# Kernel tuning notes

Hardware: AMD Instinct MI355X
Metric: run time of the kernel (lower is better)

The kernel has to match this reference:

```python
import jax, jax.numpy as jnp
import numpy as np

NUM_TOKEN = 1024
IN_DIM = 512
OUT_DIM = 512
E = 1024          # expansion_factor * in_token_dims
S = 128
EPS = 1e-5
SQRT_S = float(np.sqrt(S))


def _rope_seq(x):
    """RoPE over axis 1 (sequence), last axis is feature dim. x: [B, L, ..., D]."""
    L = x.shape[1]
    half = x.shape[-1] // 2
    pos = jnp.arange(L, dtype=jnp.float32)
    inv_freq = 10000.0 ** (jnp.arange(half, dtype=jnp.float32) / half)
    sinusoid = pos[:, None] * inv_freq[None, :]          # [L, half]
    bshape = (1, L) + (1,) * (x.ndim - 3) + (half,)
    sin = jnp.sin(sinusoid).reshape(bshape)
    cos = jnp.cos(sinusoid).reshape(bshape)
    x1, x2 = jnp.split(x, 2, axis=-1)
    return jnp.concatenate([x1 * cos - x2 * sin, x2 * cos + x1 * sin], axis=-1)


def setup_inputs() -> dict:
    key = jax.random.key(0)
    ks = jax.random.split(key, 8)
    B = 32
    x = jax.random.normal(ks[0], (B, NUM_TOKEN, IN_DIM), jnp.float32)
    uv_w = jax.random.normal(ks[1], (2 * E + S, IN_DIM), jnp.float32) / np.sqrt(IN_DIM)
    o_w = jax.random.normal(ks[2], (OUT_DIM, E), jnp.float32) / np.sqrt(E)
    gamma = jax.random.uniform(ks[3], (2, S), jnp.float32)
    beta = jax.random.uniform(ks[4], (2, S), jnp.float32)
    w = jax.random.uniform(ks[5], (2 * NUM_TOKEN - 1,), jnp.float32)
    g = jnp.ones((1,), jnp.float32)                       # ScaleNorm gain
    res_scale = jnp.ones((IN_DIM,), jnp.float32)
    layer_scale = jnp.ones((OUT_DIM,), jnp.float32)
    return dict(x=x, uv_w=uv_w, o_w=o_w, gamma=gamma, beta=beta, w=w,
                g=g, res_scale=res_scale, layer_scale=layer_scale)


def reference(x, uv_w, o_w, gamma, beta, w, g, res_scale, layer_scale):
    B, L, D = x.shape
    # ScaleNorm
    norm = jnp.linalg.norm(x, axis=-1, keepdims=True) * (D ** -0.5)
    xn = x / jnp.maximum(norm, EPS) * g
    # shift mixing (time shift: first half channels shifted right by 1 token)
    xs, xp = jnp.split(xn, 2, axis=-1)
    xs = jnp.pad(xs, ((0, 0), (1, 0), (0, 0)))[:, :L, :]
    xn = jnp.concatenate([xs, xp], axis=-1)
    # uv projection + SiLU, then split into u, v, base
    uv = jax.nn.silu(xn @ uv_w.T)                         # [B, L, 2E+S]
    u, v, base = jnp.split(uv, [E, 2 * E], axis=-1)
    # per-head affine then RoPE
    base = base[:, :, None, :] * gamma[None, None] + beta  # [B, L, 2, S]
    base = _rope_seq(base)
    q, k = base[:, :, 0, :], base[:, :, 1, :]
    qk = jnp.einsum('bls,bms->blm', q, k)                 # [B, L, L]
    # structure-mode relative position bias: bias[i, j] = w[j - i + L - 1]
    idx = jnp.arange(L)[None, :] - jnp.arange(L)[:, None] + (L - 1)
    qk = qk + w[idx][None]
    kernel = jnp.square(jax.nn.relu(qk / SQRT_S))
    out = u * jnp.einsum('blm,bme->ble', kernel, v)       # gated quadratic attn
    out = out @ o_w.T                                     # [B, L, OUT_DIM]
    return x * res_scale + out * layer_scale
```

## Files before the change

kernel.cpp:

```cpp
#include <hip/hip_runtime.h>
#include <hip/hip_bf16.h>
#include <math.h>

typedef unsigned short u16;
typedef __bf16 bf16x8 __attribute__((ext_vector_type(8)));
typedef float f32x4 __attribute__((ext_vector_type(4)));

#define NB 32
#define LSEQ 1024
#define DIN 512
#define EDIM 1024
#define SDIM 128
#define NTOK (NB * LSEQ)
#define NUV 2176
#define CHUNK 16

#define AS1 __attribute__((address_space(1)))
#define AS3 __attribute__((address_space(3)))

__device__ __forceinline__ u16 f2bf(float f) {
  unsigned u = __builtin_bit_cast(unsigned, f);
  u += 0x7fffu + ((u >> 16) & 1u);
  return (u16)(u >> 16);
}
__device__ __forceinline__ float bf2f(u16 h) {
  unsigned u = ((unsigned)h) << 16;
  return __builtin_bit_cast(float, u);
}
__device__ __forceinline__ float fast_silu(float x) {
  float t = __builtin_amdgcn_exp2f(-1.44269504088896f * x);
  return x * __builtin_amdgcn_rcpf(1.0f + t);
}


__global__ __launch_bounds__(256) void k_f32_to_bf16(const float* __restrict__ in,
                                                     u16* __restrict__ out, int n4) {
  int i = blockIdx.x * 256 + threadIdx.x;
  if (i < n4) {
    float4 f = ((const float4*)in)[i];
    ushort4 o;
    o.x = f2bf(f.x); o.y = f2bf(f.y); o.z = f2bf(f.z); o.w = f2bf(f.w);
    ((ushort4*)out)[i] = o;
  }
}

__global__ __launch_bounds__(256) void k_normshift(const float* __restrict__ x,
                                                   const float* __restrict__ g,
                                                   u16* __restrict__ xn2) {
  int t = blockIdx.x;
  int l = t & (LSEQ - 1);
  float2 v = ((const float2*)(x + (size_t)t * DIN))[threadIdx.x];
  float ss = v.x * v.x + v.y * v.y;
  for (int o = 32; o > 0; o >>= 1) ss += __shfl_down(ss, o, 64);
  __shared__ float p[4];
  if ((threadIdx.x & 63) == 0) p[threadIdx.x >> 6] = ss;
  __syncthreads();
  float s = p[0] + p[1] + p[2] + p[3];
  float norm = sqrtf(s * (1.0f / (float)DIN));
  float inv = g[0] / fmaxf(norm, 1e-5f);
  int d = threadIdx.x * 2;
  ushort2 ob; ob.x = f2bf(v.x * inv); ob.y = f2bf(v.y * inv);
  if (d >= 256) {
    *(ushort2*)(xn2 + (size_t)t * DIN + d) = ob;
  } else {
    if (l < LSEQ - 1) *(ushort2*)(xn2 + (size_t)(t + 1) * DIN + d) = ob;
    if (l == 0) { ushort2 z = {0, 0}; *(ushort2*)(xn2 + (size_t)t * DIN + d) = z; }
  }
}

__global__ __launch_bounds__(256) void k_rope_table(float* __restrict__ sin_t,
                                                    float* __restrict__ cos_t) {
  int idx = blockIdx.x * 256 + threadIdx.x;
  int l = idx >> 6, j = idx & 63;
  double freq = pow(10000.0, (double)j / 64.0);
  float arg = (float)l * (float)freq;
  double a = (double)arg;
  sin_t[idx] = (float)sin(a);
  cos_t[idx] = (float)cos(a);
}

__global__ __launch_bounds__(256) void k_qkbuild(const u16* __restrict__ base,
                                                 const float* __restrict__ gamma,
                                                 const float* __restrict__ beta,
                                                 const float* __restrict__ sin_t,
                                                 const float* __restrict__ cos_t,
                                                 u16* __restrict__ q, u16* __restrict__ k) {
  int idx = blockIdx.x * 256 + threadIdx.x;
  int t = idx >> 6, j = idx & 63;
  int l = t & (LSEQ - 1);
  float b1 = bf2f(base[(size_t)t * SDIM + j]);
  float b2 = bf2f(base[(size_t)t * SDIM + j + 64]);
  float s = sin_t[l * 64 + j], c = cos_t[l * 64 + j];
  {
    float y1 = b1 * gamma[j] + beta[j];
    float y2 = b2 * gamma[64 + j] + beta[64 + j];
    q[(size_t)t * SDIM + j]      = f2bf(y1 * c - y2 * s);
    q[(size_t)t * SDIM + j + 64] = f2bf(y2 * c + y1 * s);
  }
  {
    float y1 = b1 * gamma[128 + j] + beta[128 + j];
    float y2 = b2 * gamma[192 + j] + beta[192 + j];
    k[(size_t)t * SDIM + j]      = f2bf(y1 * c - y2 * s);
    k[(size_t)t * SDIM + j + 64] = f2bf(y2 * c + y1 * s);
  }
}


__device__ __forceinline__ void stage128x32(const u16* g, int ld, u16* l, int tid) {
  int r = tid >> 2;
  int c = ((tid & 3) ^ ((tid >> 3) & 3)) * 8;
  const u16* g0 = g + (size_t)r * ld + c;
  const u16* g1 = g + (size_t)(r + 64) * ld + c;
  u16* l0 = l + tid * 8;
  u16* l1 = l + tid * 8 + 2048;
  __builtin_amdgcn_global_load_lds((AS1 unsigned int*)g0, (AS3 unsigned int*)l0, 16, 0, 0);
  __builtin_amdgcn_global_load_lds((AS1 unsigned int*)g1, (AS3 unsigned int*)l1, 16, 0, 0);
}

__device__ __forceinline__ void gemm_core(const u16* A, const u16* B, int K,
                                          int lda, int ldb,
                                          u16* sA, u16* sB, f32x4 acc[4][4]) {
  const int tid = threadIdx.x;
  const int lane = tid & 63;
  const int wid = tid >> 6;
  const int wr = wid >> 1, wc = wid & 1;
  const int fr = lane & 15, kg = lane >> 4;
  const int ks = (kg ^ ((fr >> 1) & 3)) * 8;
  const u16* sa_base = sA + (wr * 64 + fr) * 32 + ks;
  const u16* sb_base = sB + (wc * 64 + fr) * 32 + ks;
  for (int k0 = 0; k0 < K; k0 += 32) {
    stage128x32(A + k0, lda, sA, tid);
    stage128x32(B + k0, ldb, sB, tid);
    __syncthreads();
    bf16x8 a[4], b[4];
#pragma unroll
    for (int i = 0; i < 4; ++i) a[i] = *(const bf16x8*)(sa_base + i * 16 * 32);
#pragma unroll
    for (int i = 0; i < 4; ++i) b[i] = *(const bf16x8*)(sb_base + i * 16 * 32);
#pragma unroll
    for (int m = 0; m < 4; ++m)
#pragma unroll
      for (int n = 0; n < 4; ++n)
        acc[m][n] = __builtin_amdgcn_mfma_f32_16x16x32_bf16(a[m], b[n], acc[m][n], 0, 0, 0);
    __syncthreads();
  }
}


#define GROW_A(s) (wr * 128 + (s) * 32 + wc * 8)
#define GROW_B(s) (wid * 32 + (s) * 8)

#define STG_PAIR(s, At2, Bt2, dA, dB)                                              \
  do {                                                                             \
    __builtin_amdgcn_global_load_lds(                                              \
        (AS1 unsigned int*)((At2) + (size_t)(GROW_A(s) + srow) * lda + scol),      \
        (AS3 unsigned int*)((dA) + GROW_A(s) * 64), 16, 0, 0);                     \
    __builtin_amdgcn_global_load_lds(                                              \
        (AS1 unsigned int*)((Bt2) + (size_t)(GROW_B(s) + srow) * ldb + scol),      \
        (AS3 unsigned int*)((dB) + GROW_B(s) * 64), 16, 0, 0);                     \
  } while (0)

#define RD_A(dst, cbuf, q)                                                         \
  do {                                                                             \
    _Pragma("unroll") for (int r_ = 0; r_ < 2; ++r_)                               \
    _Pragma("unroll") for (int h_ = 0; h_ < 2; ++h_)                               \
      dst[r_][h_] = *(const bf16x8*)((cbuf) + (wr * 128 + (q) * 32 + r_ * 16 + fr) * 64 + \
                                     (((h_ * 4 + kg) ^ fr7) * 8));                 \
  } while (0)

#define RD_B(cbuf)                                                                 \
  do {                                                                             \
    _Pragma("unroll") for (int n_ = 0; n_ < 4; ++n_)                               \
    _Pragma("unroll") for (int h_ = 0; h_ < 2; ++h_)                               \
      breg[n_][h_] = *(const bf16x8*)((cbuf) + (wc * 64 + n_ * 16 + fr) * 64 +     \
                                      (((h_ * 4 + kg) ^ fr7) * 8));                \
  } while (0)

#define MFMA16(s, areg)                                                            \
  do {                                                                             \
    __builtin_amdgcn_s_setprio(1);                                                 \
    _Pragma("unroll") for (int r_ = 0; r_ < 2; ++r_)                               \
    _Pragma("unroll") for (int n_ = 0; n_ < 4; ++n_)                               \
    _Pragma("unroll") for (int h_ = 0; h_ < 2; ++h_)                               \
      acc[(s) * 2 + r_][n_] = __builtin_amdgcn_mfma_f32_16x16x32_bf16(             \
          areg[r_][h_], breg[n_][h_], acc[(s) * 2 + r_][n_], 0, 0, 0);             \
    __builtin_amdgcn_s_setprio(0);                                                 \
  } while (0)

#define BAR_FENCE()                                                                \
  do { __builtin_amdgcn_s_barrier(); asm volatile("" ::: "memory"); } while (0)

__device__ __forceinline__ void gemm256p_core(const u16* __restrict__ A, int lda,
                                              const u16* __restrict__ B, int ldb,
                                              int K, u16* smem, f32x4 (&acc)[8][4]) {
  const int tid = threadIdx.x;
  const int lane = tid & 63, wid = tid >> 6;
  const int wr = wid >> 2, wc = wid & 3;
  const int fr = lane & 15, kg = lane >> 4, fr7 = fr & 7;
  const int srow = lane >> 3;
  const int scol = ((lane & 7) ^ srow) * 8;
  u16* cA = smem;
  u16* cB = smem + 16384;
  u16* nA = smem + 32768;
  u16* nB = smem + 49152;
  const int nt = K >> 6;

#pragma unroll
  for (int s = 0; s < 4; ++s) STG_PAIR(s, A, B, cA, cB);
#pragma unroll
  for (int s = 0; s < 4; ++s) STG_PAIR(s, A + 64, B + 64, nA, nB);
  asm volatile("s_waitcnt vmcnt(8)" ::: "memory");
  BAR_FENCE();

  bf16x8 breg[4][2], ac[2][2], an[2][2];
  RD_B(cB);
  RD_A(ac, cA, 0);

  for (int t = 0; t < nt; ++t) {
    const bool st = (t + 2) < nt;
    const u16* At2 = A + (size_t)(t + 2) * 64;
    const u16* Bt2 = B + (size_t)(t + 2) * 64;
    MFMA16(0, ac);
    RD_A(an, cA, 1);
    BAR_FENCE();
    if (st) STG_PAIR(0, At2, Bt2, cA, cB);
    MFMA16(1, an);
    RD_A(ac, cA, 2);
    BAR_FENCE();
    if (st) STG_PAIR(1, At2, Bt2, cA, cB);
    MFMA16(2, ac);
    RD_A(an, cA, 3);
    BAR_FENCE();
    if (st) STG_PAIR(2, At2, Bt2, cA, cB);
    MFMA16(3, an);
    if (st) asm volatile("s_waitcnt vmcnt(6)" ::: "memory");
    else    asm volatile("s_waitcnt vmcnt(0)" ::: "memory");
    BAR_FENCE();
    if (st) STG_PAIR(3, At2, Bt2, cA, cB);
    { u16* tp = cA; cA = nA; nA = tp; tp = cB; cB = nB; nB = tp; }
    if (t + 1 < nt) { RD_B(cB); RD_A(ac, cA, 0); }
  }
}


__global__ __launch_bounds__(512, 2) void k_gemm_uv(const u16* __restrict__ xn2,
                                                    const u16* __restrict__ wbf,
                                                    u16* __restrict__ u, u16* __restrict__ vt,
                                                    u16* __restrict__ base) {
  __shared__ __align__(16) u16 smem[65536];
  f32x4 acc[8][4] = {};
  int bid = blockIdx.x;
  int xcd = bid & 7;
  int off = bid >> 3;
  int m0 = (xcd * 16 + off / 9) * 256;
  int n0 = (off % 9) * 256;
  gemm256p_core(xn2 + (size_t)m0 * DIN, DIN, wbf + (size_t)n0 * DIN, DIN, DIN, smem, acc);
  int lane = threadIdx.x & 63, wid = threadIdx.x >> 6;
  int wr = wid >> 2, wc = wid & 3;
  int cb = n0 + wc * 64 + (lane & 15);
  int rb = m0 + wr * 128 + (lane >> 4) * 4;
  if (n0 < EDIM) {
#pragma unroll
    for (int mm = 0; mm < 8; ++mm)
#pragma unroll
      for (int n = 0; n < 4; ++n) {
        int c = cb + n * 16;
#pragma unroll
        for (int j = 0; j < 4; ++j) {
          int r = rb + mm * 16 + j;
          u[(size_t)r * EDIM + c] = f2bf(fast_silu(acc[mm][n][j]));
        }
      }
  } else if (n0 < 2 * EDIM) {
    int b = m0 >> 10;
    u16* vtb = vt + (size_t)b * (EDIM * LSEQ);
#pragma unroll
    for (int mm = 0; mm < 8; ++mm) {
      int l0 = (rb + mm * 16) & (LSEQ - 1);
#pragma unroll
      for (int n = 0; n < 4; ++n) {
        int e = cb + n * 16 - EDIM;
        ushort4 o;
        o.x = f2bf(fast_silu(acc[mm][n][0]));
        o.y = f2bf(fast_silu(acc[mm][n][1]));
        o.z = f2bf(fast_silu(acc[mm][n][2]));
        o.w = f2bf(fast_silu(acc[mm][n][3]));
        *(ushort4*)(vtb + (size_t)e * LSEQ + l0) = o;
      }
    }
  } else if (wc < 2) {
#pragma unroll
    for (int mm = 0; mm < 8; ++mm)
#pragma unroll
      for (int n = 0; n < 4; ++n) {
        int c = cb + n * 16 - 2 * EDIM;
#pragma unroll
        for (int j = 0; j < 4; ++j) {
          int r = rb + mm * 16 + j;
          base[(size_t)r * SDIM + c] = f2bf(fast_silu(acc[mm][n][j]));
        }
      }
  }
}

__global__ __launch_bounds__(256) void k_gemm_qk(const u16* __restrict__ q,
                                                 const u16* __restrict__ k,
                                                 const float* __restrict__ w,
                                                 u16* __restrict__ scores) {
  __shared__ __align__(16) u16 sA[4096];
  __shared__ __align__(16) u16 sB[4096];
  f32x4 acc[4][4] = {};
  int bid = blockIdx.x;
  int xcd = bid & 7;
  int off = bid >> 3;
  int b = xcd * 2 + (off >> 6);
  int t = off & 63;
  int m0 = (t >> 3) * 128, n0 = (t & 7) * 128;
  gemm_core(q + (size_t)(b * LSEQ + m0) * SDIM, k + (size_t)(b * LSEQ + n0) * SDIM,
            SDIM, SDIM, SDIM, sA, sB, acc);
  int lane = threadIdx.x & 63, wid = threadIdx.x >> 6;
  int wr = wid >> 1, wc = wid & 1;
  int cb = n0 + wc * 64 + (lane & 15);
  int rb = m0 + wr * 64 + (lane >> 4) * 4;
  const float inv_sqrt_s = 0.08838834764831845f;
  u16* sc_b = scores + (size_t)b * LSEQ * LSEQ;
#pragma unroll
  for (int m = 0; m < 4; ++m)
#pragma unroll
    for (int n = 0; n < 4; ++n) {
      int c = cb + n * 16;
#pragma unroll
      for (int j = 0; j < 4; ++j) {
        int r = rb + m * 16 + j;
        float val = (acc[m][n][j] + w[c - r + (LSEQ - 1)]) * inv_sqrt_s;
        val = fmaxf(val, 0.0f);
        sc_b[(size_t)r * LSEQ + c] = f2bf(val * val);
      }
    }
}

__global__ __launch_bounds__(512, 2) void k_gemm_pv(const u16* __restrict__ scores,
                                                    const u16* __restrict__ vt,
                                                    u16* u_io) {
  __shared__ __align__(16) u16 smem[65536];
  f32x4 acc[8][4] = {};
  int bid = blockIdx.x;
  int xcd = bid & 7;
  int off = bid >> 3;
  int b = xcd * 2 + (off >> 4);
  int t = off & 15;
  int m0 = (t >> 2) * 256, n0 = (t & 3) * 256;
  gemm256p_core(scores + (size_t)b * LSEQ * LSEQ + (size_t)m0 * LSEQ, LSEQ,
                vt + (size_t)b * LSEQ * EDIM + (size_t)n0 * LSEQ, LSEQ,
                LSEQ, smem, acc);
  int lane = threadIdx.x & 63, wid = threadIdx.x >> 6;
  int wr = wid >> 2, wc = wid & 3;
  int cb = n0 + wc * 64 + (lane & 15);
  int rb = m0 + wr * 128 + (lane >> 4) * 4;
#pragma unroll
  for (int mm = 0; mm < 8; ++mm)
#pragma unroll
    for (int n = 0; n < 4; ++n) {
      int c = cb + n * 16;
#pragma unroll
      for (int j = 0; j < 4; ++j) {
        int r = rb + mm * 16 + j;
        size_t idx = (size_t)(b * LSEQ + r) * EDIM + c;
        u_io[idx] = f2bf(acc[mm][n][j] * bf2f(u_io[idx]));
      }
    }
}

__global__ __launch_bounds__(512, 2) void k_gemm_out(const u16* __restrict__ attn,
                                                     const u16* __restrict__ owbf,
                                                     const float* __restrict__ x,
                                                     const float* __restrict__ res_scale,
                                                     const float* __restrict__ layer_scale,
                                                     float* __restrict__ out) {
  __shared__ __align__(16) u16 smem[65536];
  f32x4 acc[8][4] = {};
  int bid = blockIdx.x;
  int xcd = bid & 7;
  int off = bid >> 3;
  int m0 = (xcd * 16 + (off >> 1)) * 256;
  int n0 = (off & 1) * 256;
  gemm256p_core(attn + (size_t)m0 * EDIM, EDIM, owbf + (size_t)n0 * EDIM, EDIM,
                EDIM, smem, acc);
  int lane = threadIdx.x & 63, wid = threadIdx.x >> 6;
  int wr = wid >> 2, wc = wid & 3;
  int cb = n0 + wc * 64 + (lane & 15);
  int rb = m0 + wr * 128 + (lane >> 4) * 4;
#pragma unroll
  for (int mm = 0; mm < 8; ++mm)
#pragma unroll
    for (int n = 0; n < 4; ++n) {
      int c = cb + n * 16;
#pragma unroll
      for (int j = 0; j < 4; ++j) {
        int r = rb + mm * 16 + j;
        out[(size_t)r * DIN + c] =
            x[(size_t)r * DIN + c] * res_scale[c] + acc[mm][n][j] * layer_scale[c];
      }
    }
}


extern "C" void kernel_launch(void* const* d_in, const int* in_sizes, int n_in,
                              void* d_out, int out_size, void* d_ws, size_t ws_size,
                              hipStream_t stream) {
  const float* x          = (const float*)d_in[0];
  const float* uv_w       = (const float*)d_in[1];
  const float* o_w        = (const float*)d_in[2];
  const float* gamma      = (const float*)d_in[3];
  const float* beta       = (const float*)d_in[4];
  const float* w          = (const float*)d_in[5];
  const float* g          = (const float*)d_in[6];
  const float* res_scale  = (const float*)d_in[7];
  const float* layer_scale= (const float*)d_in[8];
  float* out = (float*)d_out;

  char* ws = (char*)d_ws;
  u16* xn2    = (u16*)(ws + 0);
  u16* q      = (u16*)(ws + 0);
  u16* k      = (u16*)(ws + 8388608);
  u16* scores = (u16*)(ws + 16777216);
  u16* base   = (u16*)(ws + 33554432);
  u16* u_io   = (u16*)(ws + 50331648);
  u16* vt     = (u16*)(ws + 117440512);
  u16* uvw_bf = (u16*)(ws + 184549376);
  u16* ow_bf  = (u16*)(ws + 186908672);
  float* sin_t = (float*)(ws + 187957248);
  float* cos_t = (float*)(ws + 188219392);

  k_f32_to_bf16<<<dim3((NUV * DIN / 4 + 255) / 256), 256, 0, stream>>>(uv_w, uvw_bf, NUV * DIN / 4);
  k_f32_to_bf16<<<dim3((DIN * EDIM / 4 + 255) / 256), 256, 0, stream>>>(o_w, ow_bf, DIN * EDIM / 4);
  k_rope_table<<<dim3(LSEQ * 64 / 256), 256, 0, stream>>>(sin_t, cos_t);
  k_normshift<<<dim3(NTOK), 256, 0, stream>>>(x, g, xn2);

  k_gemm_uv<<<dim3(1152), 512, 0, stream>>>(xn2, uvw_bf, u_io, vt, base);

  k_qkbuild<<<dim3(NTOK * 64 / 256), 256, 0, stream>>>(base, gamma, beta, sin_t, cos_t, q, k);

  for (int ch = 0; ch < NB / CHUNK; ++ch) {
    size_t tok0 = (size_t)ch * CHUNK * LSEQ;
    k_gemm_qk<<<dim3(1024), 256, 0, stream>>>(q + tok0 * SDIM, k + tok0 * SDIM, w, scores);
    k_gemm_pv<<<dim3(256), 512, 0, stream>>>(scores, vt + tok0 * EDIM, u_io + tok0 * EDIM);
  }

  k_gemm_out<<<dim3(256), 512, 0, stream>>>(u_io, ow_bf, x, res_scale, layer_scale, out);
}
```

Baseline: 318.5 us.

## Fuse QK scoring and PV into one flash-style attention kernel

Replaces the chunked two-kernel path (QK scores written to a global bf16 buffer, then a PV GEMM reading them back) with a single kernel. Each block keeps Q in registers, streams K and V^T tiles through double-buffered LDS, computes the relu-squared scores with the relative-position bias into LDS, and accumulates into the output tile. This removes the global round trip of the L×L score matrix and the extra launches. The cost is that QK is recomputed for each of the four E-tiles, and the smaller 128x256 output tile with more barriers may lower MFMA efficiency.

```diff
diff --git a/kernel.cpp b/kernel.cpp
--- a/kernel.cpp
+++ b/kernel.cpp
@@ -13,7 +13,6 @@
 #define SDIM 128
 #define NTOK (NB * LSEQ)
 #define NUV 2176
-#define CHUNK 16
 
 #define AS1 __attribute__((address_space(1)))
 #define AS3 __attribute__((address_space(3)))
@@ -106,47 +105,6 @@
 }
 
 
-__device__ __forceinline__ void stage128x32(const u16* g, int ld, u16* l, int tid) {
-  int r = tid >> 2;
-  int c = ((tid & 3) ^ ((tid >> 3) & 3)) * 8;
-  const u16* g0 = g + (size_t)r * ld + c;
-  const u16* g1 = g + (size_t)(r + 64) * ld + c;
-  u16* l0 = l + tid * 8;
-  u16* l1 = l + tid * 8 + 2048;
-  __builtin_amdgcn_global_load_lds((AS1 unsigned int*)g0, (AS3 unsigned int*)l0, 16, 0, 0);
-  __builtin_amdgcn_global_load_lds((AS1 unsigned int*)g1, (AS3 unsigned int*)l1, 16, 0, 0);
-}
-
-__device__ __forceinline__ void gemm_core(const u16* A, const u16* B, int K,
-                                          int lda, int ldb,
-                                          u16* sA, u16* sB, f32x4 acc[4][4]) {
-  const int tid = threadIdx.x;
-  const int lane = tid & 63;
-  const int wid = tid >> 6;
-  const int wr = wid >> 1, wc = wid & 1;
-  const int fr = lane & 15, kg = lane >> 4;
-  const int ks = (kg ^ ((fr >> 1) & 3)) * 8;
-  const u16* sa_base = sA + (wr * 64 + fr) * 32 + ks;
-  const u16* sb_base = sB + (wc * 64 + fr) * 32 + ks;
-  for (int k0 = 0; k0 < K; k0 += 32) {
-    stage128x32(A + k0, lda, sA, tid);
-    stage128x32(B + k0, ldb, sB, tid);
-    __syncthreads();
-    bf16x8 a[4], b[4];
-#pragma unroll
-    for (int i = 0; i < 4; ++i) a[i] = *(const bf16x8*)(sa_base + i * 16 * 32);
-#pragma unroll
-    for (int i = 0; i < 4; ++i) b[i] = *(const bf16x8*)(sb_base + i * 16 * 32);
-#pragma unroll
-    for (int m = 0; m < 4; ++m)
-#pragma unroll
-      for (int n = 0; n < 4; ++n)
-        acc[m][n] = __builtin_amdgcn_mfma_f32_16x16x32_bf16(a[m], b[n], acc[m][n], 0, 0, 0);
-    __syncthreads();
-  }
-}
-
-
 #define GROW_A(s) (wr * 128 + (s) * 32 + wc * 8)
 #define GROW_B(s) (wid * 32 + (s) * 8)
 
@@ -241,7 +199,6 @@
     if (t + 1 < nt) { RD_B(cB); RD_A(ac, cA, 0); }
   }
 }
-
 
 __global__ __launch_bounds__(512, 2) void k_gemm_uv(const u16* __restrict__ xn2,
                                                     const u16* __restrict__ wbf,
@@ -303,70 +260,149 @@
   }
 }
 
-__global__ __launch_bounds__(256) void k_gemm_qk(const u16* __restrict__ q,
-                                                 const u16* __restrict__ k,
+__global__ __launch_bounds__(512, 2) void k_attn(const u16* __restrict__ qg_,
+                                                 const u16* __restrict__ kg_,
+                                                 const u16* __restrict__ vtg,
                                                  const float* __restrict__ w,
-                                                 u16* __restrict__ scores) {
-  __shared__ __align__(16) u16 sA[4096];
-  __shared__ __align__(16) u16 sB[4096];
-  f32x4 acc[4][4] = {};
+                                                 u16* u_io) {
+  __shared__ __align__(16) u16 smem[59648];
+  u16* k0 = smem;            u16* k1 = smem + 8192;
+  u16* v0 = smem + 16384;    u16* v1 = smem + 32768;
+  u16* sS = smem + 49152;
+  float* wwin = (float*)(smem + 57344);
+
+  const int tid = threadIdx.x;
+  const int lane = tid & 63, wid = tid >> 6;
+  const int fr = lane & 15, kg = lane >> 4, fr7 = fr & 7;
   int bid = blockIdx.x;
   int xcd = bid & 7;
-  int off = bid >> 3;
-  int b = xcd * 2 + (off >> 6);
-  int t = off & 63;
-  int m0 = (t >> 3) * 128, n0 = (t & 7) * 128;
-  gemm_core(q + (size_t)(b * LSEQ + m0) * SDIM, k + (size_t)(b * LSEQ + n0) * SDIM,
-            SDIM, SDIM, SDIM, sA, sB, acc);
-  int lane = threadIdx.x & 63, wid = threadIdx.x >> 6;
-  int wr = wid >> 1, wc = wid & 1;
-  int cb = n0 + wc * 64 + (lane & 15);
-  int rb = m0 + wr * 64 + (lane >> 4) * 4;
+  int idx = bid >> 3;
+  int b = xcd * 4 + (idx >> 5);
+  int t5 = idx & 31;
+  int m0 = (t5 >> 2) * 128;
+  int e0 = (t5 & 3) * 256;
+  const u16* qp = qg_ + (size_t)(b * LSEQ) * SDIM;
+  const u16* kp = kg_ + (size_t)(b * LSEQ) * SDIM;
+  const u16* vp = vtg + (size_t)b * LSEQ * EDIM + (size_t)e0 * LSEQ;
+
+  if (tid < 288)
+    __builtin_amdgcn_global_load_lds((AS1 unsigned int*)(w + (896 - m0) + tid * 4),
+                                     (AS3 unsigned int*)(wwin + tid * 4), 16, 0, 0);
+
+  bf16x8 qreg[4];
+#pragma unroll
+  for (int kf = 0; kf < 4; ++kf)
+    qreg[kf] = *(const bf16x8*)(qp + (size_t)(m0 + wid * 16 + fr) * SDIM + kf * 32 + kg * 8);
+
+  auto stage_k = [&](const u16* src_base, u16* dst) {
+#pragma unroll
+    for (int j2 = 0; j2 < 2; ++j2) {
+      int ix = tid + j2 * 512;
+      int row = ix >> 4, slot = ix & 15;
+      int sslot = (slot & 8) | ((slot & 7) ^ (row & 7));
+      __builtin_amdgcn_global_load_lds((AS1 unsigned int*)(src_base + (size_t)row * SDIM + sslot * 8),
+                                       (AS3 unsigned int*)(dst + ix * 8), 16, 0, 0);
+    }
+  };
+  auto stage_vt = [&](const u16* src_base, u16* dst) {
+#pragma unroll
+    for (int j2 = 0; j2 < 4; ++j2) {
+      int ix = tid + j2 * 512;
+      int row = ix >> 3, slot = (ix & 7) ^ (row & 7);
+      __builtin_amdgcn_global_load_lds((AS1 unsigned int*)(src_base + (size_t)row * LSEQ + slot * 8),
+                                       (AS3 unsigned int*)(dst + ix * 8), 16, 0, 0);
+    }
+  };
+
+  stage_k(kp, k0);
+  stage_vt(vp, v0);
+  stage_k(kp + 64 * SDIM, k1);
+  stage_vt(vp + 64, v1);
+  asm volatile("s_waitcnt vmcnt(6)" ::: "memory");
+  __builtin_amdgcn_sched_barrier(0);
+  BAR_FENCE();
+
+  const int wr = wid >> 2, wc = wid & 3;
+  f32x4 acc[4][4] = {};
   const float inv_sqrt_s = 0.08838834764831845f;
-  u16* sc_b = scores + (size_t)b * LSEQ * LSEQ;
-#pragma unroll
-  for (int m = 0; m < 4; ++m)
+
+  for (int t = 0; t < 16; ++t) {
+    u16* kc = (t & 1) ? k1 : k0;
+    u16* vc = (t & 1) ? v1 : v0;
+    const bool st = t < 14;
+    int l0 = t * 64;
+    f32x4 sacc[4] = {};
+#pragma unroll
+    for (int n = 0; n < 4; ++n)
+#pragma unroll
+      for (int kf = 0; kf < 4; ++kf) {
+        int sl = kf * 4 + kg;
+        int sw = (sl & 8) | ((sl & 7) ^ fr7);
+        bf16x8 kfr = *(const bf16x8*)(kc + (n * 16 + fr) * 128 + sw * 8);
+        sacc[n] = __builtin_amdgcn_mfma_f32_16x16x32_bf16(qreg[kf], kfr, sacc[n], 0, 0, 0);
+      }
+    {
+      int mbase = wid * 16 + kg * 4;
+#pragma unroll
+      for (int n = 0; n < 4; ++n) {
+        int lloc = n * 16 + fr;
+#pragma unroll
+        for (int j = 0; j < 4; ++j) {
+          int row = mbase + j;
+          float val = (sacc[n][j] + wwin[l0 + lloc + 127 - row]) * inv_sqrt_s;
+          val = fmaxf(val, 0.0f);
+          int sw = (lloc >> 3) ^ (row & 7);
+          sS[row * 64 + sw * 8 + (lloc & 7)] = f2bf(val * val);
+        }
+      }
+    }
+    asm volatile("s_waitcnt lgkmcnt(0)" ::: "memory");
+    __builtin_amdgcn_sched_barrier(0);
+    BAR_FENCE();
+    if (st) stage_k(kp + (size_t)(l0 + 128) * SDIM, kc);
+#pragma unroll
+    for (int kh = 0; kh < 2; ++kh) {
+      bf16x8 afr[4], bfr[4];
+#pragma unroll
+      for (int i = 0; i < 4; ++i) {
+        int row = wr * 64 + i * 16 + fr;
+        int sw = (kh * 4 + kg) ^ fr7;
+        afr[i] = *(const bf16x8*)(sS + row * 64 + sw * 8);
+      }
+#pragma unroll
+      for (int n = 0; n < 4; ++n) {
+        int row = wc * 64 + n * 16 + fr;
+        int sw = (kh * 4 + kg) ^ fr7;
+        bfr[n] = *(const bf16x8*)(vc + row * 64 + sw * 8);
+      }
+      __builtin_amdgcn_s_setprio(1);
+#pragma unroll
+      for (int i = 0; i < 4; ++i)
+#pragma unroll
+        for (int n = 0; n < 4; ++n)
+          acc[i][n] = __builtin_amdgcn_mfma_f32_16x16x32_bf16(afr[i], bfr[n], acc[i][n], 0, 0, 0);
+      __builtin_amdgcn_s_setprio(0);
+    }
+    BAR_FENCE();
+    if (st) stage_vt(vp + (l0 + 128), vc);
+    if (st) asm volatile("s_waitcnt vmcnt(6)" ::: "memory");
+    else    asm volatile("s_waitcnt vmcnt(0)" ::: "memory");
+    __builtin_amdgcn_sched_barrier(0);
+    BAR_FENCE();
+  }
+
+  int cb = e0 + wc * 64 + fr;
+  int rb = m0 + wr * 64 + kg * 4;
+#pragma unroll
+  for (int i = 0; i < 4; ++i)
 #pragma unroll
     for (int n = 0; n < 4; ++n) {
       int c = cb + n * 16;
 #pragma unroll
       for (int j = 0; j < 4; ++j) {
-        int r = rb + m * 16 + j;
-        float val = (acc[m][n][j] + w[c - r + (LSEQ - 1)]) * inv_sqrt_s;
-        val = fmaxf(val, 0.0f);
-        sc_b[(size_t)r * LSEQ + c] = f2bf(val * val);
-      }
-    }
-}
-
-__global__ __launch_bounds__(512, 2) void k_gemm_pv(const u16* __restrict__ scores,
-                                                    const u16* __restrict__ vt,
-                                                    u16* u_io) {
-  __shared__ __align__(16) u16 smem[65536];
-  f32x4 acc[8][4] = {};
-  int bid = blockIdx.x;
-  int xcd = bid & 7;
-  int off = bid >> 3;
-  int b = xcd * 2 + (off >> 4);
-  int t = off & 15;
-  int m0 = (t >> 2) * 256, n0 = (t & 3) * 256;
-  gemm256p_core(scores + (size_t)b * LSEQ * LSEQ + (size_t)m0 * LSEQ, LSEQ,
-                vt + (size_t)b * LSEQ * EDIM + (size_t)n0 * LSEQ, LSEQ,
-                LSEQ, smem, acc);
-  int lane = threadIdx.x & 63, wid = threadIdx.x >> 6;
-  int wr = wid >> 2, wc = wid & 3;
-  int cb = n0 + wc * 64 + (lane & 15);
-  int rb = m0 + wr * 128 + (lane >> 4) * 4;
-#pragma unroll
-  for (int mm = 0; mm < 8; ++mm)
-#pragma unroll
-    for (int n = 0; n < 4; ++n) {
-      int c = cb + n * 16;
-#pragma unroll
-      for (int j = 0; j < 4; ++j) {
-        int r = rb + mm * 16 + j;
-        size_t idx = (size_t)(b * LSEQ + r) * EDIM + c;
-        u_io[idx] = f2bf(acc[mm][n][j] * bf2f(u_io[idx]));
+        int r = rb + i * 16 + j;
+        size_t ix = (size_t)(b * LSEQ + r) * EDIM + c;
+        u_io[ix] = f2bf(acc[i][n][j] * bf2f(u_io[ix]));
       }
     }
 }
@@ -423,7 +459,6 @@
   u16* xn2    = (u16*)(ws + 0);
   u16* q      = (u16*)(ws + 0);
   u16* k      = (u16*)(ws + 8388608);
-  u16* scores = (u16*)(ws + 16777216);
   u16* base   = (u16*)(ws + 33554432);
   u16* u_io   = (u16*)(ws + 50331648);
   u16* vt     = (u16*)(ws + 117440512);
@@ -441,11 +476,7 @@
 
   k_qkbuild<<<dim3(NTOK * 64 / 256), 256, 0, stream>>>(base, gamma, beta, sin_t, cos_t, q, k);
 
-  for (int ch = 0; ch < NB / CHUNK; ++ch) {
-    size_t tok0 = (size_t)ch * CHUNK * LSEQ;
-    k_gemm_qk<<<dim3(1024), 256, 0, stream>>>(q + tok0 * SDIM, k + tok0 * SDIM, w, scores);
-    k_gemm_pv<<<dim3(256), 512, 0, stream>>>(scores, vt + tok0 * EDIM, u_io + tok0 * EDIM);
-  }
+  k_attn<<<dim3(1024), 512, 0, stream>>>(q, k, vt, w, u_io);
 
   k_gemm_out<<<dim3(256), 512, 0, stream>>>(u_io, ow_bf, x, res_scale, layer_scale, out);
 }
```

Result: slower. 362.0 us (+13.6%).
